# Kernel tuning notes

Measured on AMD Instinct MI355X. Metric: run time of the kernel, lower is better.

Reference implementation:

```python
import jax, jax.numpy as jnp
import numpy as np

NEG_SLOPE = 0.2
BN_EPS = 1e-5

def lrelu(x):
    return jnp.where(x >= 0, x, NEG_SLOPE * x)

def setup_inputs() -> dict:
    key = jax.random.key(0)
    ks = jax.random.split(key, 12)
    B, V, D = 256, 16, 512
    s = lambda fan_in: 1.0 / np.sqrt(fan_in)
    return {
        "F": jax.random.normal(ks[0], (B, V, D), dtype=jnp.float32),
        # Relation MLP: Linear(1024,512) x3 (stored as (in,out))
        "W1": jax.random.uniform(ks[1], (2 * D, D), jnp.float32, -s(2 * D), s(2 * D)),
        "b1": jax.random.uniform(ks[2], (D,), jnp.float32, -s(2 * D), s(2 * D)),
        "W2": jax.random.uniform(ks[3], (D, D), jnp.float32, -s(D), s(D)),
        "b2": jax.random.uniform(ks[4], (D,), jnp.float32, -s(D), s(D)),
        "W3": jax.random.uniform(ks[5], (D, D), jnp.float32, -s(D), s(D)),
        "b3": jax.random.uniform(ks[6], (D,), jnp.float32, -s(D), s(D)),
        # Fusion: Linear(1024,512) + BatchNorm1d(512)
        "Wf": jax.random.uniform(ks[7], (2 * D, D), jnp.float32, -s(2 * D), s(2 * D)),
        "bf": jax.random.uniform(ks[8], (D,), jnp.float32, -s(2 * D), s(2 * D)),
        "gamma": jnp.ones((D,), jnp.float32),
        "beta": jnp.zeros((D,), jnp.float32),
    }

def reference(F, W1, b1, W2, b2, W3, b3, Wf, bf, gamma, beta):
    B, V, D = F.shape
    # All-pairs broadcast + concat -> (B, V, V, 2D)
    F_i = jnp.broadcast_to(F[:, :, None, :], (B, V, V, D))
    F_j = jnp.broadcast_to(F[:, None, :, :], (B, V, V, D))
    M = jnp.concatenate([F_i, F_j], axis=-1)
    # 3-layer Relation MLP with LeakyReLU(0.2)
    h = lrelu(M @ W1 + b1)
    h = lrelu(h @ W2 + b2)
    h = lrelu(h @ W3 + b3)
    # Sum over neighbor axis (dim -2) -> (B, V, D)
    Msum = jnp.sum(h, axis=-2)
    # Fusion: concat, Linear, BatchNorm1d (training-mode batch stats), LeakyReLU
    X = jnp.concatenate([F, Msum], axis=-1).reshape(-1, 2 * D)  # (B*V, 2D)
    y = X @ Wf + bf
    mean = jnp.mean(y, axis=0)
    var = jnp.mean(jnp.square(y - mean), axis=0)  # biased var (torch BN)
    yn = (y - mean) * jax.lax.rsqrt(var + BN_EPS) * gamma + beta
    return lrelu(yn).reshape(B, V, D)
```

## Files before the change

### kernel.cpp

```cpp
#include <hip/hip_runtime.h>

using f32x4  = __attribute__((ext_vector_type(4))) float;
using f32x16 = __attribute__((ext_vector_type(16))) float;
using bf16x8 = __attribute__((ext_vector_type(8))) __bf16;

static constexpr int DD = 512;
static constexpr int NTOK = 4096;

__device__ __forceinline__ float bf2f(unsigned short u) {
  unsigned int v = ((unsigned int)u) << 16;
  return __builtin_bit_cast(float, v);
}
__device__ __forceinline__ float bflo(unsigned int u) {
  return __builtin_bit_cast(float, u << 16);
}
__device__ __forceinline__ float bfhi(unsigned int u) {
  return __builtin_bit_cast(float, u & 0xffff0000u);
}
__device__ __forceinline__ unsigned short f2bf(float f) {
  unsigned int u = __builtin_bit_cast(unsigned int, f);
  unsigned int r = u + 0x7fffu + ((u >> 16) & 1u);
  return (unsigned short)(r >> 16);
}
__device__ __forceinline__ float lrelu(float v) { return v >= 0.f ? v : 0.2f * v; }


__global__ __launch_bounds__(256) void k_prep(const float* __restrict__ F,
                                              const float* __restrict__ W1,
                                              const float* __restrict__ W2,
                                              const float* __restrict__ W3,
                                              const float* __restrict__ Wf,
                                              unsigned short* __restrict__ XP,
                                              unsigned short* __restrict__ W1P,
                                              unsigned short* __restrict__ W2P,
                                              unsigned short* __restrict__ W3P,
                                              unsigned short* __restrict__ WfP,
                                              float* __restrict__ sums) {
  const int bid = blockIdx.x, tid = threadIdx.x;
  if (bid < 8192) {
    int idx = (bid << 8) + tid;
    int t = idx >> 9, c = idx & 511;
    XP[((t >> 4) * 32 + (c >> 5)) * 512 + ((c >> 3) & 3) * 128 + (t & 15) * 8 + (c & 7)] = f2bf(F[idx]);
  } else if (bid < 10240) {
    int idx = ((bid - 8192) << 8) + tid;
    int k = idx >> 10, n = idx & 1023;
    float v = W1[(n < 512 ? k : 512 + k) * 512 + (n & 511)];
    W1P[((n >> 4) * 16 + (k >> 5)) * 512 + ((k >> 3) & 3) * 128 + (n & 15) * 8 + (k & 7)] = f2bf(v);
  } else if (bid < 11264) {
    int idx = ((bid - 10240) << 8) + tid;
    int k = idx >> 9, n = idx & 511;
    int off = (((n >> 6) * 32 + (k >> 4)) * 2 + ((n >> 5) & 1)) * 512 +
              ((k >> 3) & 1) * 256 + (n & 31) * 8 + (k & 7);
    W2P[off] = f2bf(W2[idx]);
  } else if (bid < 12288) {
    int idx = ((bid - 11264) << 8) + tid;
    int k = idx >> 9, n = idx & 511;
    int off = (((n >> 6) * 32 + (k >> 4)) * 2 + ((n >> 5) & 1)) * 512 +
              ((k >> 3) & 1) * 256 + (n & 31) * 8 + (k & 7);
    W3P[off] = f2bf(W3[idx]);
  } else if (bid < 14336) {
    int idx = ((bid - 12288) << 8) + tid;
    int k = idx >> 9, n = idx & 511;
    WfP[((n >> 4) * 32 + (k >> 5)) * 512 + ((k >> 3) & 3) * 128 + (n & 15) * 8 + (k & 7)] = f2bf(Wf[idx]);
  } else {
    reinterpret_cast<float4*>(sums)[tid] = float4{0.f, 0.f, 0.f, 0.f};
  }
}

__global__ __launch_bounds__(512) void k_gemm_ac(const unsigned short* __restrict__ XP,
                                                 const unsigned short* __restrict__ W1P,
                                                 unsigned short* __restrict__ ACP) {
  const int tid = threadIdx.x, lane = tid & 63, wid = tid >> 6;
  const int wm = wid >> 2, wn = wid & 3;
  const int l15 = lane & 15;
  const int bx = blockIdx.x, by = blockIdx.y;

  f32x4 acc[2][4];
#pragma unroll
  for (int mt = 0; mt < 2; ++mt)
#pragma unroll
    for (int nt = 0; nt < 4; ++nt) acc[mt][nt] = f32x4{0.f, 0.f, 0.f, 0.f};

  bf16x8 ca[2], cb[4], na[2], nb[4];
  auto ldA = [&](bf16x8 (&d)[2], int ks) {
#pragma unroll
    for (int mt = 0; mt < 2; ++mt)
      d[mt] = *reinterpret_cast<const bf16x8*>(XP + (((bx * 4 + wm * 2 + mt) * 32 + ks) << 9) + lane * 8);
  };
  auto ldB = [&](bf16x8 (&d)[4], int ks) {
#pragma unroll
    for (int nt = 0; nt < 4; ++nt)
      d[nt] = *reinterpret_cast<const bf16x8*>(W1P + ((((by * 16 + wn * 4 + nt) * 16) + ks) << 9) + lane * 8);
  };

  ldA(ca, 0); ldB(cb, 0);
  for (int ks = 0; ks < 16; ++ks) {
    int kn = (ks + 1) & 15;
    ldA(na, kn); ldB(nb, kn);
    __builtin_amdgcn_s_setprio(1);
#pragma unroll
    for (int mt = 0; mt < 2; ++mt)
#pragma unroll
      for (int nt = 0; nt < 4; ++nt)
        acc[mt][nt] = __builtin_amdgcn_mfma_f32_16x16x32_bf16(ca[mt], cb[nt], acc[mt][nt], 0, 0, 0);
    __builtin_amdgcn_s_setprio(0);
#pragma unroll
    for (int q = 0; q < 2; ++q) ca[q] = na[q];
#pragma unroll
    for (int q = 0; q < 4; ++q) cb[q] = nb[q];
  }
#pragma unroll
  for (int mt = 0; mt < 2; ++mt)
#pragma unroll
    for (int nt = 0; nt < 4; ++nt) {
      int col = by * 256 + wn * 64 + nt * 16 + l15;
      int panel = bx * 4 + wm * 2 + mt;
#pragma unroll
      for (int r = 0; r < 4; ++r) {
        int rowi = (lane >> 4) * 4 + r;
        ACP[(panel * 32 + (col >> 5)) * 512 + ((col >> 3) & 3) * 128 + rowi * 8 + (col & 7)] = f2bf(acc[mt][nt][r]);
      }
    }
}

__global__ __launch_bounds__(1024, 4) void k_relation(const unsigned short* __restrict__ ACP,
                                                      const unsigned short* __restrict__ W2P,
                                                      const unsigned short* __restrict__ W3P,
                                                      const float* __restrict__ b1,
                                                      const float* __restrict__ b2,
                                                      const float* __restrict__ b3,
                                                      unsigned short* __restrict__ XP) {
  __shared__ unsigned short lds[65536];
  char* ldsb = reinterpret_cast<char*>(lds);
  const int tid = threadIdx.x;
  const int b = blockIdx.x >> 1, half = blockIdx.x & 1;

  {
    const int c8b = (tid >> 3) & 7;
    const int r = ((tid >> 6) << 3) | (tid & 7);
    const int il = r >> 4, j = r & 15;
    const int rowA = half * 8 + il;
    const int rt = r >> 5, r31 = r & 31;
#pragma unroll
    for (int it = 0; it < 8; ++it) {
      const int c8 = c8b + it * 8;
      uint4 av = *reinterpret_cast<const uint4*>(ACP + ((b * 32 + (c8 >> 2)) << 9) + (c8 & 3) * 128 + rowA * 8);
      uint4 cv = *reinterpret_cast<const uint4*>(ACP + ((b * 32 + 16 + (c8 >> 2)) << 9) + (c8 & 3) * 128 + j * 8);
      float4 bv0 = *reinterpret_cast<const float4*>(b1 + c8 * 8);
      float4 bv1 = *reinterpret_cast<const float4*>(b1 + c8 * 8 + 4);
      unsigned int au[4] = {av.x, av.y, av.z, av.w};
      unsigned int cu[4] = {cv.x, cv.y, cv.z, cv.w};
      float bb[8] = {bv0.x, bv0.y, bv0.z, bv0.w, bv1.x, bv1.y, bv1.z, bv1.w};
      unsigned int ou[4];
#pragma unroll
      for (int q = 0; q < 4; ++q) {
        float v0 = lrelu(bflo(au[q]) + bflo(cu[q]) + bb[2 * q]);
        float v1 = lrelu(bfhi(au[q]) + bfhi(cu[q]) + bb[2 * q + 1]);
        ou[q] = ((unsigned int)f2bf(v1) << 16) | (unsigned int)f2bf(v0);
      }
      uint4 o; o.x = ou[0]; o.y = ou[1]; o.z = ou[2]; o.w = ou[3];
      *reinterpret_cast<uint4*>(ldsb + (rt * 32 + (c8 >> 1)) * 1024 + (c8 & 1) * 512 + r31 * 16) = o;
    }
  }
  __syncthreads();

  const int lane = tid & 63, wid = tid >> 6;
  const int r31 = lane & 31, h = lane >> 5;
  const int fg = wid >> 1;
  const int rg = wid & 1;

  const unsigned short* w2base = W2P + (fg << 15) + lane * 8;
  const unsigned short* w3base = W3P + (fg << 15) + lane * 8;
  const unsigned short* lrd = lds + (rg * 2) * 32 * 512 + lane * 8;

  f32x16 acc[2][2];
  bf16x8 aA[2], aB[2], bA[2], bB[2];

  auto ldA_ = [&](bf16x8 (&d)[2], const unsigned short* __restrict__ wb, int ks) {
    d[0] = *reinterpret_cast<const bf16x8*>(wb + ks * 1024);
    d[1] = *reinterpret_cast<const bf16x8*>(wb + ks * 1024 + 512);
  };
  auto ldB_ = [&](bf16x8 (&d)[2], int ks) {
    d[0] = *reinterpret_cast<const bf16x8*>(lrd + ks * 512);
    d[1] = *reinterpret_cast<const bf16x8*>(lrd + 32 * 512 + ks * 512);
  };

  auto layer = [&](const unsigned short* __restrict__ wb) {
#pragma unroll
    for (int mt = 0; mt < 2; ++mt)
#pragma unroll
      for (int nt = 0; nt < 2; ++nt)
#pragma unroll
        for (int e = 0; e < 16; ++e) acc[mt][nt][e] = 0.f;
    ldA_(aA, wb, 0); ldB_(bA, 0);
#pragma unroll 1
    for (int ks = 0; ks < 32; ks += 2) {
      ldA_(aB, wb, ks + 1); ldB_(bB, ks + 1);
      __builtin_amdgcn_s_setprio(1);
      acc[0][0] = __builtin_amdgcn_mfma_f32_32x32x16_bf16(aA[0], bA[0], acc[0][0], 0, 0, 0);
      acc[0][1] = __builtin_amdgcn_mfma_f32_32x32x16_bf16(aA[0], bA[1], acc[0][1], 0, 0, 0);
      acc[1][0] = __builtin_amdgcn_mfma_f32_32x32x16_bf16(aA[1], bA[0], acc[1][0], 0, 0, 0);
      acc[1][1] = __builtin_amdgcn_mfma_f32_32x32x16_bf16(aA[1], bA[1], acc[1][1], 0, 0, 0);
      __builtin_amdgcn_s_setprio(0);
      const int ksn = (ks + 2) & 31;
      ldA_(aA, wb, ksn); ldB_(bA, ksn);
      __builtin_amdgcn_s_setprio(1);
      acc[0][0] = __builtin_amdgcn_mfma_f32_32x32x16_bf16(aB[0], bB[0], acc[0][0], 0, 0, 0);
      acc[0][1] = __builtin_amdgcn_mfma_f32_32x32x16_bf16(aB[0], bB[1], acc[0][1], 0, 0, 0);
      acc[1][0] = __builtin_amdgcn_mfma_f32_32x32x16_bf16(aB[1], bB[0], acc[1][0], 0, 0, 0);
      acc[1][1] = __builtin_amdgcn_mfma_f32_32x32x16_bf16(aB[1], bB[1], acc[1][1], 0, 0, 0);
      __builtin_amdgcn_s_setprio(0);
    }
  };

  auto store_h = [&](const float* __restrict__ bias) {
#pragma unroll
    for (int mt = 0; mt < 2; ++mt)
#pragma unroll
      for (int g = 0; g < 4; ++g) {
        float4 bv = *reinterpret_cast<const float4*>(bias + fg * 64 + mt * 32 + g * 8 + h * 4);
        const int ks16 = fg * 4 + mt * 2 + (g >> 1);
        const int kh = g & 1;
#pragma unroll
        for (int nt = 0; nt < 2; ++nt) {
          unsigned int w0 = f2bf(lrelu(acc[mt][nt][4 * g + 0] + bv.x));
          unsigned int w1 = f2bf(lrelu(acc[mt][nt][4 * g + 1] + bv.y));
          unsigned int w2 = f2bf(lrelu(acc[mt][nt][4 * g + 2] + bv.z));
          unsigned int w3 = f2bf(lrelu(acc[mt][nt][4 * g + 3] + bv.w));
          uint2 val; val.x = (w1 << 16) | w0; val.y = (w3 << 16) | w2;
          *reinterpret_cast<uint2*>(ldsb + ((rg * 2 + nt) * 32 + ks16) * 1024 + kh * 512 + r31 * 16 + h * 8) = val;
        }
      }
  };

  layer(w2base);
  __syncthreads();
  store_h(b2);
  __syncthreads();
  layer(w3base);
  __syncthreads();
  store_h(b3);
  __syncthreads();

  if (wid < 8) {
    const int t = wid;
    const int o = lane;
    const char* base = ldsb + ((t >> 1) * 32 + (o >> 1)) * 1024 + (o & 1) * 512 + (t & 1) * 256;
    float s[8] = {0.f, 0.f, 0.f, 0.f, 0.f, 0.f, 0.f, 0.f};
#pragma unroll
    for (int it = 0; it < 16; ++it) {
      int j = (it + o) & 15;
      uint4 v = *reinterpret_cast<const uint4*>(base + j * 16);
      s[0] += bflo(v.x); s[1] += bfhi(v.x);
      s[2] += bflo(v.y); s[3] += bfhi(v.y);
      s[4] += bflo(v.z); s[5] += bfhi(v.z);
      s[6] += bflo(v.w); s[7] += bfhi(v.w);
    }
    uint4 o4;
    o4.x = ((unsigned int)f2bf(s[1]) << 16) | f2bf(s[0]);
    o4.y = ((unsigned int)f2bf(s[3]) << 16) | f2bf(s[2]);
    o4.z = ((unsigned int)f2bf(s[5]) << 16) | f2bf(s[4]);
    o4.w = ((unsigned int)f2bf(s[7]) << 16) | f2bf(s[6]);
    int tg15 = half * 8 + t;
    *reinterpret_cast<uint4*>(XP + ((b * 32 + 16 + (o >> 2)) << 9) + (o & 3) * 128 + tg15 * 8) = o4;
  }
}

__global__ __launch_bounds__(512) void k_fusion(const unsigned short* __restrict__ XP,
                                                const unsigned short* __restrict__ WfP,
                                                const float* __restrict__ bfv,
                                                float* __restrict__ y,
                                                float* __restrict__ sums,
                                                float* __restrict__ sumsq) {
  const int tid = threadIdx.x, lane = tid & 63, wid = tid >> 6;
  const int wm = wid >> 2, wn = wid & 3;
  const int l15 = lane & 15;
  const int bx = blockIdx.x, by = blockIdx.y;
  const int rowbase = bx * 64 + wm * 32;
  const int colbase = by * 128 + wn * 32;

  f32x4 acc[2][2];
#pragma unroll
  for (int mt = 0; mt < 2; ++mt)
#pragma unroll
    for (int nt = 0; nt < 2; ++nt) acc[mt][nt] = f32x4{0.f, 0.f, 0.f, 0.f};

  bf16x8 ca[2], cb[2], na[2], nb[2];
  auto ldA = [&](bf16x8 (&d)[2], int ks) {
#pragma unroll
    for (int mt = 0; mt < 2; ++mt)
      d[mt] = *reinterpret_cast<const bf16x8*>(XP + (((bx * 4 + wm * 2 + mt) * 32 + ks) << 9) + lane * 8);
  };
  auto ldB = [&](bf16x8 (&d)[2], int ks) {
#pragma unroll
    for (int nt = 0; nt < 2; ++nt)
      d[nt] = *reinterpret_cast<const bf16x8*>(WfP + (((by * 8 + wn * 2 + nt) * 32 + ks) << 9) + lane * 8);
  };

  ldA(ca, 0); ldB(cb, 0);
  for (int ks = 0; ks < 32; ++ks) {
    int kn = (ks + 1) & 31;
    ldA(na, kn); ldB(nb, kn);
    __builtin_amdgcn_s_setprio(1);
#pragma unroll
    for (int mt = 0; mt < 2; ++mt)
#pragma unroll
      for (int nt = 0; nt < 2; ++nt)
        acc[mt][nt] = __builtin_amdgcn_mfma_f32_16x16x32_bf16(ca[mt], cb[nt], acc[mt][nt], 0, 0, 0);
    __builtin_amdgcn_s_setprio(0);
#pragma unroll
    for (int q = 0; q < 2; ++q) { ca[q] = na[q]; cb[q] = nb[q]; }
  }

  float s[2] = {0.f, 0.f}, q2[2] = {0.f, 0.f};
#pragma unroll
  for (int nt = 0; nt < 2; ++nt) {
    int col = colbase + nt * 16 + l15;
    float bias = bfv[col];
#pragma unroll
    for (int mt = 0; mt < 2; ++mt)
#pragma unroll
      for (int r = 0; r < 4; ++r) {
        int row = rowbase + mt * 16 + (lane >> 4) * 4 + r;
        float v = acc[mt][nt][r] + bias;
        y[row * DD + col] = v;
        s[nt] += v; q2[nt] += v * v;
      }
  }
#pragma unroll
  for (int nt = 0; nt < 2; ++nt) {
    s[nt] += __shfl_xor(s[nt], 16);  s[nt] += __shfl_xor(s[nt], 32);
    q2[nt] += __shfl_xor(q2[nt], 16); q2[nt] += __shfl_xor(q2[nt], 32);
    if (lane < 16) {
      int col = colbase + nt * 16 + l15;
      atomicAdd(&sums[col], s[nt]);
      atomicAdd(&sumsq[col], q2[nt]);
    }
  }
}

__global__ __launch_bounds__(256) void k_bnapply(const float* __restrict__ y,
                                                 const float* __restrict__ sums,
                                                 const float* __restrict__ sumsq,
                                                 const float* __restrict__ gamma,
                                                 const float* __restrict__ beta,
                                                 float* __restrict__ out) {
  int idx = blockIdx.x * 256 + threadIdx.x;
  if (idx >= NTOK * DD) return;
  int c = idx & 511;
  float mean = sums[c] * (1.0f / 4096.0f);
  float var = sumsq[c] * (1.0f / 4096.0f) - mean * mean;
  float rstd = rsqrtf(var + 1e-5f);
  float v = (y[idx] - mean) * rstd * gamma[c] + beta[c];
  out[idx] = lrelu(v);
}

extern "C" void kernel_launch(void* const* d_in, const int* in_sizes, int n_in,
                              void* d_out, int out_size, void* d_ws, size_t ws_size,
                              hipStream_t stream) {
  const float* F   = (const float*)d_in[0];
  const float* W1  = (const float*)d_in[1];
  const float* b1  = (const float*)d_in[2];
  const float* W2  = (const float*)d_in[3];
  const float* b2  = (const float*)d_in[4];
  const float* W3  = (const float*)d_in[5];
  const float* b3  = (const float*)d_in[6];
  const float* Wf  = (const float*)d_in[7];
  const float* bfv = (const float*)d_in[8];
  const float* gamma = (const float*)d_in[9];
  const float* beta  = (const float*)d_in[10];
  float* out = (float*)d_out;

  char* ws = (char*)d_ws;
  unsigned short* XP  = (unsigned short*)(ws);
  unsigned short* ACP = (unsigned short*)(ws + (8u << 20));
  unsigned short* W1P = (unsigned short*)(ws + (16u << 20));
  unsigned short* W2P = (unsigned short*)(ws + (17u << 20));
  unsigned short* W3P = (unsigned short*)(ws + (17u << 20) + (512u << 10));
  unsigned short* WfP = (unsigned short*)(ws + (18u << 20));
  float* y            = (float*)(ws + (19u << 20));
  float* sums         = (float*)(ws + (27u << 20));
  float* sumsq        = sums + 512;

  k_prep<<<14337, 256, 0, stream>>>(F, W1, W2, W3, Wf, XP, W1P, W2P, W3P, WfP, sums);
  k_gemm_ac<<<dim3(64, 4), 512, 0, stream>>>(XP, W1P, ACP);
  k_relation<<<512, 1024, 0, stream>>>(ACP, W2P, W3P, b1, b2, b3, XP);
  k_fusion<<<dim3(64, 4), 512, 0, stream>>>(XP, WfP, bfv, y, sums, sumsq);
  k_bnapply<<<(NTOK * DD + 255) / 256, 256, 0, stream>>>(y, sums, sumsq, gamma, beta, out);
}
```

Before: 126.7 us.

## Halve relation block to 8 waves, stage weights to LDS via async global_load_lds

The relation kernel now runs 512 threads per block. Each wave covers all 128 pair rows (4 n-tiles) instead of 64, so each weight fragment is reused across twice as many MFMAs. W2/W3 slices are double-buffered into LDS with global_load_lds, and the loop waits with explicit vmcnt counts so weight fetches overlap compute. The packed weight layout is reorganised to be k-major for these contiguous async loads. Each thread now holds twice as many accumulator registers, LDS use grows to 160KB per block, and the hand-written vmcnt waits carry a correctness risk.

```diff
diff --git a/kernel.cpp b/kernel.cpp
--- a/kernel.cpp
+++ b/kernel.cpp
@@ -49,14 +49,12 @@
   } else if (bid < 11264) {
     int idx = ((bid - 10240) << 8) + tid;
     int k = idx >> 9, n = idx & 511;
-    int off = (((n >> 6) * 32 + (k >> 4)) * 2 + ((n >> 5) & 1)) * 512 +
-              ((k >> 3) & 1) * 256 + (n & 31) * 8 + (k & 7);
+    int off = (k >> 4) * 8192 + (n >> 5) * 512 + ((k >> 3) & 1) * 256 + (n & 31) * 8 + (k & 7);
     W2P[off] = f2bf(W2[idx]);
   } else if (bid < 12288) {
     int idx = ((bid - 11264) << 8) + tid;
     int k = idx >> 9, n = idx & 511;
-    int off = (((n >> 6) * 32 + (k >> 4)) * 2 + ((n >> 5) & 1)) * 512 +
-              ((k >> 3) & 1) * 256 + (n & 31) * 8 + (k & 7);
+    int off = (k >> 4) * 8192 + (n >> 5) * 512 + ((k >> 3) & 1) * 256 + (n & 31) * 8 + (k & 7);
     W3P[off] = f2bf(W3[idx]);
   } else if (bid < 14336) {
     int idx = ((bid - 12288) << 8) + tid;
@@ -123,27 +121,27 @@
     }
 }
 
-__global__ __launch_bounds__(1024, 4) void k_relation(const unsigned short* __restrict__ ACP,
-                                                      const unsigned short* __restrict__ W2P,
-                                                      const unsigned short* __restrict__ W3P,
-                                                      const float* __restrict__ b1,
-                                                      const float* __restrict__ b2,
-                                                      const float* __restrict__ b3,
-                                                      unsigned short* __restrict__ XP) {
-  __shared__ unsigned short lds[65536];
+__global__ __launch_bounds__(512, 2) void k_relation(const unsigned short* __restrict__ ACP,
+                                                     const unsigned short* __restrict__ W2P,
+                                                     const unsigned short* __restrict__ W3P,
+                                                     const float* __restrict__ b1,
+                                                     const float* __restrict__ b2,
+                                                     const float* __restrict__ b3,
+                                                     unsigned short* __restrict__ XP) {
+  __shared__ unsigned short lds[81920];
   char* ldsb = reinterpret_cast<char*>(lds);
+  unsigned short* wbuf = lds + 65536;
   const int tid = threadIdx.x;
   const int b = blockIdx.x >> 1, half = blockIdx.x & 1;
 
   {
-    const int c8b = (tid >> 3) & 7;
-    const int r = ((tid >> 6) << 3) | (tid & 7);
+    const int r = tid >> 2;
     const int il = r >> 4, j = r & 15;
     const int rowA = half * 8 + il;
     const int rt = r >> 5, r31 = r & 31;
 #pragma unroll
-    for (int it = 0; it < 8; ++it) {
-      const int c8 = c8b + it * 8;
+    for (int it = 0; it < 16; ++it) {
+      const int c8 = (tid & 3) + it * 4;
       uint4 av = *reinterpret_cast<const uint4*>(ACP + ((b * 32 + (c8 >> 2)) << 9) + (c8 & 3) * 128 + rowA * 8);
       uint4 cv = *reinterpret_cast<const uint4*>(ACP + ((b * 32 + 16 + (c8 >> 2)) << 9) + (c8 & 3) * 128 + j * 8);
       float4 bv0 = *reinterpret_cast<const float4*>(b1 + c8 * 8);
@@ -164,53 +162,67 @@
   }
   __syncthreads();
 
-  const int lane = tid & 63, wid = tid >> 6;
+  const int lane = tid & 63, fg = tid >> 6;
   const int r31 = lane & 31, h = lane >> 5;
-  const int fg = wid >> 1;
-  const int rg = wid & 1;
-
-  const unsigned short* w2base = W2P + (fg << 15) + lane * 8;
-  const unsigned short* w3base = W3P + (fg << 15) + lane * 8;
-  const unsigned short* lrd = lds + (rg * 2) * 32 * 512 + lane * 8;
-
-  f32x16 acc[2][2];
-  bf16x8 aA[2], aB[2], bA[2], bB[2];
-
-  auto ldA_ = [&](bf16x8 (&d)[2], const unsigned short* __restrict__ wb, int ks) {
-    d[0] = *reinterpret_cast<const bf16x8*>(wb + ks * 1024);
-    d[1] = *reinterpret_cast<const bf16x8*>(wb + ks * 1024 + 512);
-  };
-  auto ldB_ = [&](bf16x8 (&d)[2], int ks) {
-    d[0] = *reinterpret_cast<const bf16x8*>(lrd + ks * 512);
-    d[1] = *reinterpret_cast<const bf16x8*>(lrd + 32 * 512 + ks * 512);
-  };
-
-  auto layer = [&](const unsigned short* __restrict__ wb) {
-#pragma unroll
-    for (int mt = 0; mt < 2; ++mt)
-#pragma unroll
-      for (int nt = 0; nt < 2; ++nt)
+
+  auto stageW = [&](const unsigned short* __restrict__ WP, int ks, int bufsel) {
+#pragma unroll
+    for (int mt = 0; mt < 2; ++mt) {
+      const unsigned short* src = WP + ks * 8192 + (fg * 2 + mt) * 512 + lane * 8;
+      unsigned short* dst = wbuf + (fg * 4 + bufsel * 2 + mt) * 512;
+      __builtin_amdgcn_global_load_lds((const __attribute__((address_space(1))) unsigned int*)src,
+                                       (__attribute__((address_space(3))) unsigned int*)dst, 16, 0, 0);
+    }
+  };
+
+  f32x16 acc[2][4];
+
+#define LDW(bufsel, mt) (*reinterpret_cast<const bf16x8*>(wbuf + (fg * 4 + (bufsel) * 2 + (mt)) * 512 + lane * 8))
+#define LDH(nt, ks) (*reinterpret_cast<const bf16x8*>(ldsb + (((nt) * 32 + (ks)) << 10) + lane * 16))
+
+  auto body = [&](int ks, int bufsel) {
+    bf16x8 w0 = LDW(bufsel, 0), w1 = LDW(bufsel, 1);
+    bf16x8 h0 = LDH(0, ks), h1 = LDH(1, ks), h2 = LDH(2, ks), h3 = LDH(3, ks);
+    __builtin_amdgcn_s_setprio(1);
+    acc[0][0] = __builtin_amdgcn_mfma_f32_32x32x16_bf16(w0, h0, acc[0][0], 0, 0, 0);
+    acc[0][1] = __builtin_amdgcn_mfma_f32_32x32x16_bf16(w0, h1, acc[0][1], 0, 0, 0);
+    acc[0][2] = __builtin_amdgcn_mfma_f32_32x32x16_bf16(w0, h2, acc[0][2], 0, 0, 0);
+    acc[0][3] = __builtin_amdgcn_mfma_f32_32x32x16_bf16(w0, h3, acc[0][3], 0, 0, 0);
+    acc[1][0] = __builtin_amdgcn_mfma_f32_32x32x16_bf16(w1, h0, acc[1][0], 0, 0, 0);
+    acc[1][1] = __builtin_amdgcn_mfma_f32_32x32x16_bf16(w1, h1, acc[1][1], 0, 0, 0);
+    acc[1][2] = __builtin_amdgcn_mfma_f32_32x32x16_bf16(w1, h2, acc[1][2], 0, 0, 0);
+    acc[1][3] = __builtin_amdgcn_mfma_f32_32x32x16_bf16(w1, h3, acc[1][3], 0, 0, 0);
+    __builtin_amdgcn_s_setprio(0);
+  };
+
+  auto kloop = [&](const unsigned short* __restrict__ WP) {
+#pragma unroll
+    for (int mt = 0; mt < 2; ++mt)
+#pragma unroll
+      for (int nt = 0; nt < 4; ++nt)
 #pragma unroll
         for (int e = 0; e < 16; ++e) acc[mt][nt][e] = 0.f;
-    ldA_(aA, wb, 0); ldB_(bA, 0);
+    stageW(WP, 0, 0);
+    stageW(WP, 1, 1);
 #pragma unroll 1
-    for (int ks = 0; ks < 32; ks += 2) {
-      ldA_(aB, wb, ks + 1); ldB_(bB, ks + 1);
-      __builtin_amdgcn_s_setprio(1);
-      acc[0][0] = __builtin_amdgcn_mfma_f32_32x32x16_bf16(aA[0], bA[0], acc[0][0], 0, 0, 0);
-      acc[0][1] = __builtin_amdgcn_mfma_f32_32x32x16_bf16(aA[0], bA[1], acc[0][1], 0, 0, 0);
-      acc[1][0] = __builtin_amdgcn_mfma_f32_32x32x16_bf16(aA[1], bA[0], acc[1][0], 0, 0, 0);
-      acc[1][1] = __builtin_amdgcn_mfma_f32_32x32x16_bf16(aA[1], bA[1], acc[1][1], 0, 0, 0);
-      __builtin_amdgcn_s_setprio(0);
-      const int ksn = (ks + 2) & 31;
-      ldA_(aA, wb, ksn); ldB_(bA, ksn);
-      __builtin_amdgcn_s_setprio(1);
-      acc[0][0] = __builtin_amdgcn_mfma_f32_32x32x16_bf16(aB[0], bB[0], acc[0][0], 0, 0, 0);
-      acc[0][1] = __builtin_amdgcn_mfma_f32_32x32x16_bf16(aB[0], bB[1], acc[0][1], 0, 0, 0);
-      acc[1][0] = __builtin_amdgcn_mfma_f32_32x32x16_bf16(aB[1], bB[0], acc[1][0], 0, 0, 0);
-      acc[1][1] = __builtin_amdgcn_mfma_f32_32x32x16_bf16(aB[1], bB[1], acc[1][1], 0, 0, 0);
-      __builtin_amdgcn_s_setprio(0);
-    }
+    for (int ks = 0; ks < 28; ks += 2) {
+      asm volatile("s_waitcnt vmcnt(2)" ::: "memory");
+      body(ks, 0);
+      stageW(WP, ks + 2, 0);
+      asm volatile("s_waitcnt vmcnt(2)" ::: "memory");
+      body(ks + 1, 1);
+      stageW(WP, ks + 3, 1);
+    }
+    asm volatile("s_waitcnt vmcnt(2)" ::: "memory");
+    body(28, 0);
+    stageW(WP, 30, 0);
+    asm volatile("s_waitcnt vmcnt(2)" ::: "memory");
+    body(29, 1);
+    stageW(WP, 31, 1);
+    asm volatile("s_waitcnt vmcnt(2)" ::: "memory");
+    body(30, 0);
+    asm volatile("s_waitcnt vmcnt(0)" ::: "memory");
+    body(31, 1);
   };
 
   auto store_h = [&](const float* __restrict__ bias) {
@@ -222,28 +234,28 @@
         const int ks16 = fg * 4 + mt * 2 + (g >> 1);
         const int kh = g & 1;
 #pragma unroll
-        for (int nt = 0; nt < 2; ++nt) {
+        for (int nt = 0; nt < 4; ++nt) {
           unsigned int w0 = f2bf(lrelu(acc[mt][nt][4 * g + 0] + bv.x));
           unsigned int w1 = f2bf(lrelu(acc[mt][nt][4 * g + 1] + bv.y));
           unsigned int w2 = f2bf(lrelu(acc[mt][nt][4 * g + 2] + bv.z));
           unsigned int w3 = f2bf(lrelu(acc[mt][nt][4 * g + 3] + bv.w));
           uint2 val; val.x = (w1 << 16) | w0; val.y = (w3 << 16) | w2;
-          *reinterpret_cast<uint2*>(ldsb + ((rg * 2 + nt) * 32 + ks16) * 1024 + kh * 512 + r31 * 16 + h * 8) = val;
+          *reinterpret_cast<uint2*>(ldsb + (nt * 32 + ks16) * 1024 + kh * 512 + r31 * 16 + h * 8) = val;
         }
       }
   };
 
-  layer(w2base);
+  kloop(W2P);
   __syncthreads();
   store_h(b2);
   __syncthreads();
-  layer(w3base);
+  kloop(W3P);
   __syncthreads();
   store_h(b3);
   __syncthreads();
 
-  if (wid < 8) {
-    const int t = wid;
+  {
+    const int t = fg;
     const int o = lane;
     const char* base = ldsb + ((t >> 1) * 32 + (o >> 1)) * 1024 + (o & 1) * 512 + (t & 1) * 256;
     float s[8] = {0.f, 0.f, 0.f, 0.f, 0.f, 0.f, 0.f, 0.f};
@@ -384,7 +396,7 @@
 
   k_prep<<<14337, 256, 0, stream>>>(F, W1, W2, W3, Wf, XP, W1P, W2P, W3P, WfP, sums);
   k_gemm_ac<<<dim3(64, 4), 512, 0, stream>>>(XP, W1P, ACP);
-  k_relation<<<512, 1024, 0, stream>>>(ACP, W2P, W3P, b1, b2, b3, XP);
+  k_relation<<<512, 512, 0, stream>>>(ACP, W2P, W3P, b1, b2, b3, XP);
   k_fusion<<<dim3(64, 4), 512, 0, stream>>>(XP, WfP, bfv, y, sums, sumsq);
   k_bnapply<<<(NTOK * DD + 255) / 256, 256, 0, stream>>>(y, sums, sumsq, gamma, beta, out);
 }
```

Measured after the change: 130.2 us. +2.8%, slower.

## Split relation blocks into quarters with 64-row tiles and smaller per-wave MFMA tiles

Applied to the files above, without the earlier changes.

The relation-MLP kernel now handles a quarter of each batch's pair rows (64 rows) per block instead of half (128 rows). This halves LDS use and doubles the grid. Each of the 16 waves now owns a 32-feature slice with two 32x32 accumulators instead of a 2x2 tile, and the W2/W3 packing is changed to match. The aim is higher occupancy (launch bound raised to 8) and more blocks in flight. The cost is that weights are reloaded from global memory twice as often, with less register reuse per loaded operand and no double-buffering of LDS operands.

```diff
diff --git a/kernel.cpp b/kernel.cpp
--- a/kernel.cpp
+++ b/kernel.cpp
@@ -7,10 +7,6 @@
 static constexpr int DD = 512;
 static constexpr int NTOK = 4096;
 
-__device__ __forceinline__ float bf2f(unsigned short u) {
-  unsigned int v = ((unsigned int)u) << 16;
-  return __builtin_bit_cast(float, v);
-}
 __device__ __forceinline__ float bflo(unsigned int u) {
   return __builtin_bit_cast(float, u << 16);
 }
@@ -49,14 +45,12 @@
   } else if (bid < 11264) {
     int idx = ((bid - 10240) << 8) + tid;
     int k = idx >> 9, n = idx & 511;
-    int off = (((n >> 6) * 32 + (k >> 4)) * 2 + ((n >> 5) & 1)) * 512 +
-              ((k >> 3) & 1) * 256 + (n & 31) * 8 + (k & 7);
+    int off = ((n >> 5) * 32 + (k >> 4)) * 512 + ((k >> 3) & 1) * 256 + (n & 31) * 8 + (k & 7);
     W2P[off] = f2bf(W2[idx]);
   } else if (bid < 12288) {
     int idx = ((bid - 11264) << 8) + tid;
     int k = idx >> 9, n = idx & 511;
-    int off = (((n >> 6) * 32 + (k >> 4)) * 2 + ((n >> 5) & 1)) * 512 +
-              ((k >> 3) & 1) * 256 + (n & 31) * 8 + (k & 7);
+    int off = ((n >> 5) * 32 + (k >> 4)) * 512 + ((k >> 3) & 1) * 256 + (n & 31) * 8 + (k & 7);
     W3P[off] = f2bf(W3[idx]);
   } else if (bid < 14336) {
     int idx = ((bid - 12288) << 8) + tid;
@@ -123,27 +117,27 @@
     }
 }
 
-__global__ __launch_bounds__(1024, 4) void k_relation(const unsigned short* __restrict__ ACP,
+__global__ __launch_bounds__(1024, 8) void k_relation(const unsigned short* __restrict__ ACP,
                                                       const unsigned short* __restrict__ W2P,
                                                       const unsigned short* __restrict__ W3P,
                                                       const float* __restrict__ b1,
                                                       const float* __restrict__ b2,
                                                       const float* __restrict__ b3,
                                                       unsigned short* __restrict__ XP) {
-  __shared__ unsigned short lds[65536];
+  __shared__ unsigned short lds[32768];
   char* ldsb = reinterpret_cast<char*>(lds);
   const int tid = threadIdx.x;
-  const int b = blockIdx.x >> 1, half = blockIdx.x & 1;
+  const int b = blockIdx.x >> 2, quarter = blockIdx.x & 3;
 
   {
-    const int c8b = (tid >> 3) & 7;
-    const int r = ((tid >> 6) << 3) | (tid & 7);
+    const int r = tid & 63;
+    const int w16 = tid >> 6;
     const int il = r >> 4, j = r & 15;
-    const int rowA = half * 8 + il;
+    const int rowA = quarter * 4 + il;
     const int rt = r >> 5, r31 = r & 31;
 #pragma unroll
-    for (int it = 0; it < 8; ++it) {
-      const int c8 = c8b + it * 8;
+    for (int it = 0; it < 4; ++it) {
+      const int c8 = w16 + it * 16;
       uint4 av = *reinterpret_cast<const uint4*>(ACP + ((b * 32 + (c8 >> 2)) << 9) + (c8 & 3) * 128 + rowA * 8);
       uint4 cv = *reinterpret_cast<const uint4*>(ACP + ((b * 32 + 16 + (c8 >> 2)) << 9) + (c8 & 3) * 128 + j * 8);
       float4 bv0 = *reinterpret_cast<const float4*>(b1 + c8 * 8);
@@ -164,86 +158,67 @@
   }
   __syncthreads();
 
-  const int lane = tid & 63, wid = tid >> 6;
+  const int lane = tid & 63, fg = tid >> 6;
   const int r31 = lane & 31, h = lane >> 5;
-  const int fg = wid >> 1;
-  const int rg = wid & 1;
-
-  const unsigned short* w2base = W2P + (fg << 15) + lane * 8;
-  const unsigned short* w3base = W3P + (fg << 15) + lane * 8;
-  const unsigned short* lrd = lds + (rg * 2) * 32 * 512 + lane * 8;
-
-  f32x16 acc[2][2];
-  bf16x8 aA[2], aB[2], bA[2], bB[2];
-
-  auto ldA_ = [&](bf16x8 (&d)[2], const unsigned short* __restrict__ wb, int ks) {
-    d[0] = *reinterpret_cast<const bf16x8*>(wb + ks * 1024);
-    d[1] = *reinterpret_cast<const bf16x8*>(wb + ks * 1024 + 512);
-  };
-  auto ldB_ = [&](bf16x8 (&d)[2], int ks) {
-    d[0] = *reinterpret_cast<const bf16x8*>(lrd + ks * 512);
-    d[1] = *reinterpret_cast<const bf16x8*>(lrd + 32 * 512 + ks * 512);
-  };
-
-  auto layer = [&](const unsigned short* __restrict__ wb) {
-#pragma unroll
-    for (int mt = 0; mt < 2; ++mt)
-#pragma unroll
-      for (int nt = 0; nt < 2; ++nt)
-#pragma unroll
-        for (int e = 0; e < 16; ++e) acc[mt][nt][e] = 0.f;
-    ldA_(aA, wb, 0); ldB_(bA, 0);
+
+  const unsigned short* w2b = W2P + (fg << 14) + lane * 8;
+  const unsigned short* w3b = W3P + (fg << 14) + lane * 8;
+
+  f32x16 acc0, acc1;
+
+  auto kloop = [&](const unsigned short* __restrict__ wb) {
+#pragma unroll
+    for (int e = 0; e < 16; ++e) { acc0[e] = 0.f; acc1[e] = 0.f; }
+    bf16x8 w = *reinterpret_cast<const bf16x8*>(wb);
 #pragma unroll 1
-    for (int ks = 0; ks < 32; ks += 2) {
-      ldA_(aB, wb, ks + 1); ldB_(bB, ks + 1);
+    for (int ks = 0; ks < 32; ++ks) {
+      bf16x8 wn = *reinterpret_cast<const bf16x8*>(wb + (ks + 1) * 512);
+      bf16x8 h0 = *reinterpret_cast<const bf16x8*>(lds + (ks << 9) + lane * 8);
+      bf16x8 h1 = *reinterpret_cast<const bf16x8*>(lds + ((32 + ks) << 9) + lane * 8);
       __builtin_amdgcn_s_setprio(1);
-      acc[0][0] = __builtin_amdgcn_mfma_f32_32x32x16_bf16(aA[0], bA[0], acc[0][0], 0, 0, 0);
-      acc[0][1] = __builtin_amdgcn_mfma_f32_32x32x16_bf16(aA[0], bA[1], acc[0][1], 0, 0, 0);
-      acc[1][0] = __builtin_amdgcn_mfma_f32_32x32x16_bf16(aA[1], bA[0], acc[1][0], 0, 0, 0);
-      acc[1][1] = __builtin_amdgcn_mfma_f32_32x32x16_bf16(aA[1], bA[1], acc[1][1], 0, 0, 0);
+      acc0 = __builtin_amdgcn_mfma_f32_32x32x16_bf16(w, h0, acc0, 0, 0, 0);
+      acc1 = __builtin_amdgcn_mfma_f32_32x32x16_bf16(w, h1, acc1, 0, 0, 0);
       __builtin_amdgcn_s_setprio(0);
-      const int ksn = (ks + 2) & 31;
-      ldA_(aA, wb, ksn); ldB_(bA, ksn);
-      __builtin_amdgcn_s_setprio(1);
-      acc[0][0] = __builtin_amdgcn_mfma_f32_32x32x16_bf16(aB[0], bB[0], acc[0][0], 0, 0, 0);
-      acc[0][1] = __builtin_amdgcn_mfma_f32_32x32x16_bf16(aB[0], bB[1], acc[0][1], 0, 0, 0);
-      acc[1][0] = __builtin_amdgcn_mfma_f32_32x32x16_bf16(aB[1], bB[0], acc[1][0], 0, 0, 0);
-      acc[1][1] = __builtin_amdgcn_mfma_f32_32x32x16_bf16(aB[1], bB[1], acc[1][1], 0, 0, 0);
-      __builtin_amdgcn_s_setprio(0);
+      w = wn;
     }
   };
 
   auto store_h = [&](const float* __restrict__ bias) {
 #pragma unroll
-    for (int mt = 0; mt < 2; ++mt)
-#pragma unroll
-      for (int g = 0; g < 4; ++g) {
-        float4 bv = *reinterpret_cast<const float4*>(bias + fg * 64 + mt * 32 + g * 8 + h * 4);
-        const int ks16 = fg * 4 + mt * 2 + (g >> 1);
-        const int kh = g & 1;
-#pragma unroll
-        for (int nt = 0; nt < 2; ++nt) {
-          unsigned int w0 = f2bf(lrelu(acc[mt][nt][4 * g + 0] + bv.x));
-          unsigned int w1 = f2bf(lrelu(acc[mt][nt][4 * g + 1] + bv.y));
-          unsigned int w2 = f2bf(lrelu(acc[mt][nt][4 * g + 2] + bv.z));
-          unsigned int w3 = f2bf(lrelu(acc[mt][nt][4 * g + 3] + bv.w));
-          uint2 val; val.x = (w1 << 16) | w0; val.y = (w3 << 16) | w2;
-          *reinterpret_cast<uint2*>(ldsb + ((rg * 2 + nt) * 32 + ks16) * 1024 + kh * 512 + r31 * 16 + h * 8) = val;
-        }
-      }
-  };
-
-  layer(w2base);
+    for (int g = 0; g < 4; ++g) {
+      float4 bv = *reinterpret_cast<const float4*>(bias + fg * 32 + g * 8 + h * 4);
+      const int ks = fg * 2 + (g >> 1);
+      const int kh = g & 1;
+      {
+        unsigned int w0 = f2bf(lrelu(acc0[4 * g + 0] + bv.x));
+        unsigned int w1 = f2bf(lrelu(acc0[4 * g + 1] + bv.y));
+        unsigned int w2 = f2bf(lrelu(acc0[4 * g + 2] + bv.z));
+        unsigned int w3 = f2bf(lrelu(acc0[4 * g + 3] + bv.w));
+        uint2 val; val.x = (w1 << 16) | w0; val.y = (w3 << 16) | w2;
+        *reinterpret_cast<uint2*>(ldsb + (0 * 32 + ks) * 1024 + kh * 512 + r31 * 16 + h * 8) = val;
+      }
+      {
+        unsigned int w0 = f2bf(lrelu(acc1[4 * g + 0] + bv.x));
+        unsigned int w1 = f2bf(lrelu(acc1[4 * g + 1] + bv.y));
+        unsigned int w2 = f2bf(lrelu(acc1[4 * g + 2] + bv.z));
+        unsigned int w3 = f2bf(lrelu(acc1[4 * g + 3] + bv.w));
+        uint2 val; val.x = (w1 << 16) | w0; val.y = (w3 << 16) | w2;
+        *reinterpret_cast<uint2*>(ldsb + (1 * 32 + ks) * 1024 + kh * 512 + r31 * 16 + h * 8) = val;
+      }
+    }
+  };
+
+  kloop(w2b);
   __syncthreads();
   store_h(b2);
   __syncthreads();
-  layer(w3base);
+  kloop(w3b);
   __syncthreads();
   store_h(b3);
   __syncthreads();
 
-  if (wid < 8) {
-    const int t = wid;
+  if (fg < 4) {
+    const int t = fg;
     const int o = lane;
     const char* base = ldsb + ((t >> 1) * 32 + (o >> 1)) * 1024 + (o & 1) * 512 + (t & 1) * 256;
     float s[8] = {0.f, 0.f, 0.f, 0.f, 0.f, 0.f, 0.f, 0.f};
@@ -261,7 +236,7 @@
     o4.y = ((unsigned int)f2bf(s[3]) << 16) | f2bf(s[2]);
     o4.z = ((unsigned int)f2bf(s[5]) << 16) | f2bf(s[4]);
     o4.w = ((unsigned int)f2bf(s[7]) << 16) | f2bf(s[6]);
-    int tg15 = half * 8 + t;
+    int tg15 = quarter * 4 + t;
     *reinterpret_cast<uint4*>(XP + ((b * 32 + 16 + (o >> 2)) << 9) + (o & 3) * 128 + tg15 * 8) = o4;
   }
 }
@@ -384,7 +359,7 @@
 
   k_prep<<<14337, 256, 0, stream>>>(F, W1, W2, W3, Wf, XP, W1P, W2P, W3P, WfP, sums);
   k_gemm_ac<<<dim3(64, 4), 512, 0, stream>>>(XP, W1P, ACP);
-  k_relation<<<512, 1024, 0, stream>>>(ACP, W2P, W3P, b1, b2, b3, XP);
+  k_relation<<<1024, 1024, 0, stream>>>(ACP, W2P, W3P, b1, b2, b3, XP);
   k_fusion<<<dim3(64, 4), 512, 0, stream>>>(XP, WfP, bfv, y, sums, sumsq);
   k_bnapply<<<(NTOK * DD + 255) / 256, 256, 0, stream>>>(y, sums, sumsq, gamma, beta, out);
 }
```

After: 138.7 us. 1.1x slower.
